# Optimization experiments

Measured on AMD Instinct MI355X. Metric: run time of the kernel, lower is better.

The kernel has to match this reference:

```python
import jax, jax.numpy as jnp
import numpy as np


def setup_inputs() -> dict:
    key = jax.random.key(0)
    k1, k2 = jax.random.split(key)
    B, H, W, N = 4, 1080, 1920, 33
    image = jax.random.uniform(k1, (B, 3, H, W), dtype=jnp.float32)
    lut = jax.random.normal(k2, (B, 3, N, N, N), dtype=jnp.float32)
    return {"image": image, "lut": lut}


def _trilinear_lut(image, lut):
    # image: (B,3,H,W) in [0,1]; lut: (B,3,N,N,N) laid out as (B, C, D, Hd, Wd)
    # grid_sample mapping: grid x<-R indexes Wd, y<-G indexes Hd, z<-B indexes D.
    # align_corners=True: unnormalized coord = ((2v-1)+1)/2*(N-1) = v*(N-1)
    # padding_mode='border': clamp coords to [0, N-1].
    B, C, H, W = image.shape
    N = lut.shape[-1]
    coords = image.reshape(B, 3, H * W) * (N - 1)          # (B,3,HW)
    coords = jnp.clip(coords, 0.0, N - 1.0)
    x, y, z = coords[:, 0], coords[:, 1], coords[:, 2]      # each (B,HW)

    def split(v):
        v0 = jnp.floor(v)
        w = v - v0                                          # frac weight
        i0 = v0.astype(jnp.int32)
        i1 = jnp.minimum(i0 + 1, N - 1)
        return i0, i1, w

    x0, x1, wx = split(x)
    y0, y1, wy = split(y)
    z0, z1, wz = split(z)

    lut_flat = lut.reshape(B, 3, N * N * N)                 # (B,3,N^3)

    def gather(zi, yi, xi):
        idx = (zi * N + yi) * N + xi                        # (B,HW)
        idx3 = jnp.broadcast_to(idx[:, None, :], (B, 3, idx.shape[-1]))
        return jnp.take_along_axis(lut_flat, idx3, axis=2)  # (B,3,HW)

    wx_ = wx[:, None, :]
    wy_ = wy[:, None, :]
    wz_ = wz[:, None, :]

    c00 = gather(z0, y0, x0) * (1 - wx_) + gather(z0, y0, x1) * wx_
    c01 = gather(z0, y1, x0) * (1 - wx_) + gather(z0, y1, x1) * wx_
    c10 = gather(z1, y0, x0) * (1 - wx_) + gather(z1, y0, x1) * wx_
    c11 = gather(z1, y1, x0) * (1 - wx_) + gather(z1, y1, x1) * wx_

    c0 = c00 * (1 - wy_) + c01 * wy_
    c1 = c10 * (1 - wy_) + c11 * wy_
    out = c0 * (1 - wz_) + c1 * wz_                         # (B,3,HW)
    return out.reshape(B, C, H, W)


def reference(image, lut):
    return _trilinear_lut(image, lut)
```

## Files before the change

kernel.cpp:

```cpp
#include <hip/hip_runtime.h>

#define BB   4
#define NN   33
#define HH   1080
#define WW   1920
#define HW   (HH * WW)
#define NNN  (NN * NN * NN)

#define TAB_PAD (NNN + NN * NN + NN + 1)

typedef float    floatx4 __attribute__((ext_vector_type(4)));


__global__ __launch_bounds__(1024) void lut_fused_kernel(const float* __restrict__ img,
                                                         const float* __restrict__ lut,
                                                         float* __restrict__ out) {
    __shared__ unsigned sml[TAB_PAD];
    __shared__ float    smax[16];

    int b   = blockIdx.x & 3;
    int blk = blockIdx.x >> 2;
    int tid = threadIdx.x;

    const float* lb = lut + (size_t)b * 3 * NNN;

    float m = 0.0f;
    for (int j = tid; j < 3 * NNN; j += 1024)
        m = fmaxf(m, fabsf(lb[j]));
#pragma unroll
    for (int off = 32; off; off >>= 1)
        m = fmaxf(m, __shfl_down(m, off, 64));
    if ((tid & 63) == 0) smax[tid >> 6] = m;
    __syncthreads();
    float bm = smax[0];
#pragma unroll
    for (int w = 1; w < 16; ++w) bm = fmaxf(bm, smax[w]);

    bm = fmaxf(bm, 1e-20f);
    int ex = (int)((__float_as_uint(bm) >> 23) & 255) - 126;
    int k  = 9 - ex;
    k = max(-120, min(120, k));
    float sp = __uint_as_float((unsigned)(127 + k) << 23);
    if (bm * sp > 511.49f) {
        k -= 1;
        sp = __uint_as_float((unsigned)(127 + k) << 23);
    }
    float sd = __uint_as_float((unsigned)(127 - k) << 23);
    float nb = -512.0f * sd;

    for (int v = tid; v < NNN; v += 1024) {
        int qr = max(-511, min(511, (int)rintf(lb[v]           * sp)));
        int qg = max(-511, min(511, (int)rintf(lb[v + NNN]     * sp)));
        int qb = max(-511, min(511, (int)rintf(lb[v + 2 * NNN] * sp)));
        sml[v] = (unsigned)(qr + 512)
               | ((unsigned)(qg + 512) << 10)
               | ((unsigned)(qb + 512) << 20);
    }
    for (int j = NNN + tid; j < TAB_PAD; j += 1024) sml[j] = 0u;
    __syncthreads();

    const float* ib = img + (size_t)b * 3 * HW;
    float*       ob = out + (size_t)b * 3 * HW;

    int g0 = blk * 8100;
    int q  = g0 + tid;

    floatx4 xs = __builtin_nontemporal_load((const floatx4*)(ib) + q);
    floatx4 ys = __builtin_nontemporal_load((const floatx4*)(ib + HW) + q);
    floatx4 zs = __builtin_nontemporal_load((const floatx4*)(ib + 2 * HW) + q);

    for (int it = 0; it < 8; ++it) {
        floatx4 nxs, nys, nzs;
        int qn = q + 1024;
        if (it < 7) {
            bool vn = (it < 6) | (tid < 8100 - 7 * 1024);
            if (vn) {
                nxs = __builtin_nontemporal_load((const floatx4*)(ib) + qn);
                nys = __builtin_nontemporal_load((const floatx4*)(ib + HW) + qn);
                nzs = __builtin_nontemporal_load((const floatx4*)(ib + 2 * HW) + qn);
            }
        }

        if ((it < 7) | (tid < 8100 - 7 * 1024)) {
            float xr[4] = {xs.x, xs.y, xs.z, xs.w};
            float yr[4] = {ys.x, ys.y, ys.z, ys.w};
            float zr[4] = {zs.x, zs.y, zs.z, zs.w};

            float rr[4], gg[4], bb[4];
#pragma unroll
            for (int i = 0; i < 4; ++i) {
                float x = fminf(fmaxf(xr[i] * 32.0f, 0.0f), 32.0f);
                float y = fminf(fmaxf(yr[i] * 32.0f, 0.0f), 32.0f);
                float z = fminf(fmaxf(zr[i] * 32.0f, 0.0f), 32.0f);
                float fx = floorf(x), fy = floorf(y), fz = floorf(z);
                float wx = x - fx, wy = y - fy, wz = z - fz;
                int a  = ((int)fz * NN + (int)fy) * NN + (int)fx;
                int a2 = a + NN * NN;

                unsigned d000 = sml[a],            d100 = sml[a + 1];
                unsigned d010 = sml[a + NN],       d110 = sml[a + NN + 1];
                unsigned d001 = sml[a2],           d101 = sml[a2 + 1];
                unsigned d011 = sml[a2 + NN],      d111 = sml[a2 + NN + 1];

                float iwx = 1.0f - wx, iwy = 1.0f - wy, iwz = 1.0f - wz;
                float a00 = iwy * iwz, a10 = wy * iwz;
                float a01 = iwy * wz,  a11 = wy * wz;
                float w000 = a00 * iwx, w100 = a00 * wx;
                float w010 = a10 * iwx, w110 = a10 * wx;
                float w001 = a01 * iwx, w101 = a01 * wx;
                float w011 = a11 * iwx, w111 = a11 * wx;

                float tr = 0.0f, tg = 0.0f, tv = 0.0f;
                auto acc = [&](unsigned d, float w) {
                    tr = fmaf(w, (float)(d & 1023u), tr);
                    tg = fmaf(w, (float)((d >> 10) & 1023u), tg);
                    tv = fmaf(w, (float)((d >> 20) & 1023u), tv);
                };
                acc(d000, w000); acc(d100, w100);
                acc(d010, w010); acc(d110, w110);
                acc(d001, w001); acc(d101, w101);
                acc(d011, w011); acc(d111, w111);

                rr[i] = fmaf(tr, sd, nb);
                gg[i] = fmaf(tg, sd, nb);
                bb[i] = fmaf(tv, sd, nb);
            }

            floatx4 ro = {rr[0], rr[1], rr[2], rr[3]};
            floatx4 go = {gg[0], gg[1], gg[2], gg[3]};
            floatx4 bo = {bb[0], bb[1], bb[2], bb[3]};
            __builtin_nontemporal_store(ro, (floatx4*)(ob) + q);
            __builtin_nontemporal_store(go, (floatx4*)(ob + HW) + q);
            __builtin_nontemporal_store(bo, (floatx4*)(ob + 2 * HW) + q);
        }

        xs = nxs; ys = nys; zs = nzs;
        q = qn;
    }
}

extern "C" void kernel_launch(void* const* d_in, const int* in_sizes, int n_in,
                              void* d_out, int out_size, void* d_ws, size_t ws_size,
                              hipStream_t stream) {
    const float* img = (const float*)d_in[0];
    const float* lut = (const float*)d_in[1];
    float* out = (float*)d_out;

    lut_fused_kernel<<<256, 1024, 0, stream>>>(img, lut, out);
}
```

Before: 210.0 us.

## Split LUT max reduction across blocks with cooperative grid sync

Each block previously read its batch's whole LUT to find the max magnitude. Now the 64 blocks per batch each reduce one slice, publish partial maxima to scratch, and combine them after a cooperative grid barrier. The LUT quantisation loop is unrolled, the clamp uses a med3 builtin, and a non-cooperative fallback path remains. The grid sync and the scratch round trip add cost and depend on all 256 blocks being co-resident.

```diff
diff --git a/kernel.cpp b/kernel.cpp
--- a/kernel.cpp
+++ b/kernel.cpp
@@ -1,4 +1,7 @@
 #include <hip/hip_runtime.h>
+#include <hip/hip_cooperative_groups.h>
+
+namespace cg = cooperative_groups;
 
 #define BB   4
 #define NN   33
@@ -6,15 +9,26 @@
 #define WW   1920
 #define HW   (HH * WW)
 #define NNN  (NN * NN * NN)
+#define TOT3 (3 * NNN)
+#define SLICE 1685
 
 #define TAB_PAD (NNN + NN * NN + NN + 1)
 
-typedef float    floatx4 __attribute__((ext_vector_type(4)));
-
-
+typedef float floatx4 __attribute__((ext_vector_type(4)));
+
+__device__ __forceinline__ float clamp32(float v) {
+#if __has_builtin(__builtin_amdgcn_fmed3f)
+    return __builtin_amdgcn_fmed3f(v, 0.0f, 32.0f);
+#else
+    return fminf(fmaxf(v, 0.0f), 32.0f);
+#endif
+}
+
+template <bool COOP>
 __global__ __launch_bounds__(1024) void lut_fused_kernel(const float* __restrict__ img,
                                                          const float* __restrict__ lut,
-                                                         float* __restrict__ out) {
+                                                         float* __restrict__ out,
+                                                         float* __restrict__ scratch) {
     __shared__ unsigned sml[TAB_PAD];
     __shared__ float    smax[16];
 
@@ -22,19 +36,54 @@
     int blk = blockIdx.x >> 2;
     int tid = threadIdx.x;
 
-    const float* lb = lut + (size_t)b * 3 * NNN;
-
-    float m = 0.0f;
-    for (int j = tid; j < 3 * NNN; j += 1024)
-        m = fmaxf(m, fabsf(lb[j]));
-#pragma unroll
-    for (int off = 32; off; off >>= 1)
-        m = fmaxf(m, __shfl_down(m, off, 64));
-    if ((tid & 63) == 0) smax[tid >> 6] = m;
-    __syncthreads();
-    float bm = smax[0];
-#pragma unroll
-    for (int w = 1; w < 16; ++w) bm = fmaxf(bm, smax[w]);
+    const float* lb = lut + (size_t)b * TOT3;
+
+    float bm;
+    if (COOP) {
+        int start = blk * SLICE;
+        int end   = min(start + SLICE, TOT3);
+        float m = 0.0f;
+        for (int j = start + tid; j < end; j += 1024)
+            m = fmaxf(m, fabsf(lb[j]));
+#pragma unroll
+        for (int off = 32; off; off >>= 1)
+            m = fmaxf(m, __shfl_down(m, off, 64));
+        if ((tid & 63) == 0) smax[tid >> 6] = m;
+        __syncthreads();
+        if (tid == 0) {
+            float pm = smax[0];
+#pragma unroll
+            for (int w = 1; w < 16; ++w) pm = fmaxf(pm, smax[w]);
+            scratch[blockIdx.x] = pm;
+        }
+
+        cg::this_grid().sync();
+
+        if (tid < 64) {
+            float pm = scratch[b + 4 * tid];
+#pragma unroll
+            for (int off = 32; off; off >>= 1)
+                pm = fmaxf(pm, __shfl_down(pm, off, 64));
+            if (tid == 0) smax[0] = pm;
+        }
+        __syncthreads();
+        bm = smax[0];
+    } else {
+        float m = 0.0f;
+#pragma unroll 8
+        for (int k = 0; k < 105; ++k)
+            m = fmaxf(m, fabsf(lb[tid + (k << 10)]));
+        if (tid < TOT3 - 105 * 1024)
+            m = fmaxf(m, fabsf(lb[tid + 105 * 1024]));
+#pragma unroll
+        for (int off = 32; off; off >>= 1)
+            m = fmaxf(m, __shfl_down(m, off, 64));
+        if ((tid & 63) == 0) smax[tid >> 6] = m;
+        __syncthreads();
+        bm = smax[0];
+#pragma unroll
+        for (int w = 1; w < 16; ++w) bm = fmaxf(bm, smax[w]);
+    }
 
     bm = fmaxf(bm, 1e-20f);
     int ex = (int)((__float_as_uint(bm) >> 23) & 255) - 126;
@@ -48,10 +97,27 @@
     float sd = __uint_as_float((unsigned)(127 - k) << 23);
     float nb = -512.0f * sd;
 
-    for (int v = tid; v < NNN; v += 1024) {
-        int qr = max(-511, min(511, (int)rintf(lb[v]           * sp)));
-        int qg = max(-511, min(511, (int)rintf(lb[v + NNN]     * sp)));
-        int qb = max(-511, min(511, (int)rintf(lb[v + 2 * NNN] * sp)));
+#pragma unroll 5
+    for (int kk = 0; kk < 35; ++kk) {
+        int v = tid + (kk << 10);
+        float r  = lb[v];
+        float g  = lb[v + NNN];
+        float bl = lb[v + 2 * NNN];
+        int qr = max(-511, min(511, (int)rintf(r  * sp)));
+        int qg = max(-511, min(511, (int)rintf(g  * sp)));
+        int qb = max(-511, min(511, (int)rintf(bl * sp)));
+        sml[v] = (unsigned)(qr + 512)
+               | ((unsigned)(qg + 512) << 10)
+               | ((unsigned)(qb + 512) << 20);
+    }
+    if (tid < NNN - 35 * 1024) {
+        int v = tid + 35 * 1024;
+        float r  = lb[v];
+        float g  = lb[v + NNN];
+        float bl = lb[v + 2 * NNN];
+        int qr = max(-511, min(511, (int)rintf(r  * sp)));
+        int qg = max(-511, min(511, (int)rintf(g  * sp)));
+        int qb = max(-511, min(511, (int)rintf(bl * sp)));
         sml[v] = (unsigned)(qr + 512)
                | ((unsigned)(qg + 512) << 10)
                | ((unsigned)(qb + 512) << 20);
@@ -89,9 +155,9 @@
             float rr[4], gg[4], bb[4];
 #pragma unroll
             for (int i = 0; i < 4; ++i) {
-                float x = fminf(fmaxf(xr[i] * 32.0f, 0.0f), 32.0f);
-                float y = fminf(fmaxf(yr[i] * 32.0f, 0.0f), 32.0f);
-                float z = fminf(fmaxf(zr[i] * 32.0f, 0.0f), 32.0f);
+                float x = clamp32(xr[i] * 32.0f);
+                float y = clamp32(yr[i] * 32.0f);
+                float z = clamp32(zr[i] * 32.0f);
                 float fx = floorf(x), fy = floorf(y), fz = floorf(z);
                 float wx = x - fx, wy = y - fy, wz = z - fz;
                 int a  = ((int)fz * NN + (int)fy) * NN + (int)fx;
@@ -145,6 +211,12 @@
     const float* img = (const float*)d_in[0];
     const float* lut = (const float*)d_in[1];
     float* out = (float*)d_out;
-
-    lut_fused_kernel<<<256, 1024, 0, stream>>>(img, lut, out);
+    float* scratch = (float*)d_ws;
+
+    void* args[] = {(void*)&img, (void*)&lut, (void*)&out, (void*)&scratch};
+    hipError_t err = hipLaunchCooperativeKernel(
+        (void*)lut_fused_kernel<true>, dim3(256), dim3(1024), args, 0, stream);
+    if (err != hipSuccess) {
+        lut_fused_kernel<false><<<256, 1024, 0, stream>>>(img, lut, out, scratch);
+    }
 }
```

Result: slower. 246.5 us (+17.4%).
